# Performance work log

Hardware: AMD Instinct MI355X
Metric: run time of the kernel (lower is better)

Reference implementation:

```python
import jax, jax.numpy as jnp
import numpy as np

N, D, YD, L = 500000, 256, 50, 1000


def setup_inputs() -> dict:
    key = jax.random.key(0)
    k_x, k_l, k_y, k_w1, k_w2 = jax.random.split(key, 5)
    lim1 = 1.0 / np.sqrt(D)
    return {
        "x": jax.random.normal(k_x, (N, D), dtype=jnp.float32),
        "labels": jax.random.randint(k_l, (N,), 0, L, dtype=jnp.int32),
        "y": jax.random.uniform(k_y, (N, YD), dtype=jnp.float32),
        "w1": jax.random.uniform(k_w1, (D, 1), jnp.float32, -lim1, lim1),
        "b1": jnp.zeros((1,), jnp.float32),
        "w2": jax.random.uniform(k_w2, (D, YD), jnp.float32, -lim1, lim1),
        "b2": jnp.zeros((YD,), jnp.float32),
        "num_labels": L,
    }


def reference(x, labels, y, w1, b1, w2, b2, num_labels):
    # sigmoid-gated features: a = sigmoid(x @ w1 + b1) * x   [N, D]
    a = jax.nn.sigmoid(x @ w1 + b1) * x
    # segment counts per label (labels assumed dense 0..L-1, all present)
    counts = jax.ops.segment_sum(jnp.ones((x.shape[0],), x.dtype), labels,
                                 num_segments=num_labels)
    denom = jnp.maximum(counts, 1.0)[:, None]  # guard empty segments
    # segment mean of gated features  [L, D]
    res = jax.ops.segment_sum(a, labels, num_segments=num_labels) / denom
    # softmax(linear2(res))  [L, YD]
    prediction = jax.nn.softmax(res @ w2 + b2, axis=1)
    # segment mean of soft targets  [L, YD]
    y_mean = jax.ops.segment_sum(y, labels, num_segments=num_labels) / denom
    # torch CrossEntropyLoss with probability targets applies log_softmax
    # to its input (here: already-softmaxed prediction) -- faithful double softmax
    logp = jax.nn.log_softmax(prediction, axis=1)
    return -jnp.mean(jnp.sum(y_mean * logp, axis=1))
```

## Files before the change

### kernel.cpp

```cpp
#include <hip/hip_runtime.h>
#include <math.h>

#define NROWS 500000
#define DIM 256
#define YDIM 50
#define NLAB 1000

#define XT 64
#define NTX ((NROWS + XT - 1) / XT)
#define XBLOCKS 256
#define ASTRIDE 264
#define ZC 51

#define YT 128
#define NTY ((NROWS + YT - 1) / YT)
#define YBLOCKS 256

typedef __attribute__((ext_vector_type(8))) short frag_ab;
typedef __attribute__((ext_vector_type(4))) float frag_cd;

__device__ __forceinline__ float b2f(unsigned short u) {
    return __uint_as_float(((unsigned)u) << 16);
}
__device__ __forceinline__ unsigned short f2b(float f) {
    unsigned u = __float_as_uint(f);
    return (unsigned short)((u + 0x7fffu + ((u >> 16) & 1u)) >> 16);
}
__device__ __forceinline__ unsigned cvt_pk_bf16(float lo, float hi) {
    unsigned r;
    asm("v_cvt_pk_bf16_f32 %0, %1, %2" : "=v"(r) : "v"(lo), "v"(hi));
    return r;
}
__device__ __forceinline__ void bar_lds() {
    asm volatile("s_waitcnt lgkmcnt(0)\n\ts_barrier" ::: "memory");
}

__global__ __launch_bounds__(1024) void k_xstream(
    const float* __restrict__ x, const int* __restrict__ labels,
    const float* __restrict__ w1, const float* __restrict__ b1,
    const float* __restrict__ w2, unsigned short* __restrict__ zpart,
    float* __restrict__ out)
{
    __shared__ __align__(16) unsigned short sA[XT * ASTRIDE];
    __shared__ __align__(16) float zst[XT][52];
    __shared__ __align__(16) unsigned short accz[NLAB * YDIM];
    __shared__ int slab[2][XT];

    const int tid = threadIdx.x, lane = tid & 63, wib = tid >> 6;
    const int bid = blockIdx.x;
    const int mh = wib >> 2, jt = wib & 3;
    const int half = lane >> 5, li = lane & 31;

    if (bid == 0 && tid == 0) out[0] = 0.0f;
    for (int k = tid; k < NLAB * YDIM / 2; k += 1024)
        reinterpret_cast<unsigned*>(accz)[k] = 0u;

    frag_ab bfr[8];
    {
        const int n = 16 * jt + (lane & 15);
        #pragma unroll
        for (int s = 0; s < 8; ++s) {
            const int k0 = 32 * s + (lane >> 4) * 8;
            #pragma unroll
            for (int i = 0; i < 8; ++i) {
                const int kk = k0 + i;
                float v = 0.f;
                if (n < YDIM)       v = w2[kk * YDIM + n];
                else if (n == YDIM) v = w1[kk];
                bfr[s][i] = (short)f2b(v);
            }
        }
    }
    const float b1v = b1[0];
    __syncthreads();

    auto PREF = [&](int t, float4* r) {
        #pragma unroll
        for (int k = 0; k < 4; ++k) {
            const int rg = t * XT + 4 * wib + k;
            r[k] = (rg < NROWS)
                 ? reinterpret_cast<const float4*>(x)[(size_t)rg * 64 + lane]
                 : make_float4(0.f, 0.f, 0.f, 0.f);
        }
    };
    auto LLAB = [&](int t) -> int {
        const int rg = t * XT + tid;
        return (tid < XT && rg < NROWS) ? labels[rg] : 0;
    };

    auto process = [&](int pft, float4* r, int& lb, int par) {
        if (tid < XT) slab[par][tid] = lb;
        uint2 pk[4];
        #pragma unroll
        for (int k = 0; k < 4; ++k) {
            pk[k].x = cvt_pk_bf16(r[k].x, r[k].y);
            pk[k].y = cvt_pk_bf16(r[k].z, r[k].w);
        }
        PREF(pft, r);
        lb = LLAB(pft);
        const int row = 4 * wib;
        #pragma unroll
        for (int k = 0; k < 4; ++k)
            *reinterpret_cast<uint2*>(&sA[(row + k) * ASTRIDE + lane * 4]) = pk[k];
        bar_lds();

        frag_cd c = {0.f, 0.f, 0.f, 0.f};
        #pragma unroll
        for (int s = 0; s < 8; ++s) {
            frag_ab a = *reinterpret_cast<const frag_ab*>(
                &sA[(16 * mh + (lane & 15)) * ASTRIDE + 32 * s + (lane >> 4) * 8]);
            c = __builtin_amdgcn_mfma_f32_16x16x32_bf16(a, bfr[s], c, 0, 0, 0);
        }
        const int zr = 16 * mh + (lane >> 4) * 4;
        const int zc = 16 * jt + (lane & 15);
        if (zc < ZC) {
            zst[zr + 0][zc] = c[0]; zst[zr + 1][zc] = c[1];
            zst[zr + 2][zc] = c[2]; zst[zr + 3][zc] = c[3];
        }
        bar_lds();

        {
            const int lbl_lane = slab[par][lane];
            unsigned long long mask = __ballot((lbl_lane & 15) == wib);
            while (mask) {
                const int ra = __builtin_ctzll(mask);
                mask &= mask - 1;
                int rb = -1;
                if (mask) { rb = __builtin_ctzll(mask); mask &= mask - 1; }
                const int r2 = (half && rb >= 0) ? rb : ra;
                const int lbv = __shfl(lbl_lane, r2);
                const float d = zst[r2][YDIM];
                const bool act = (half == 0) || (rb >= 0);
                if (act && li < 25) {
                    const float g = 1.0f / (1.0f + __expf(-(d + b1v)));
                    const float2 zv =
                        *reinterpret_cast<const float2*>(&zst[r2][2 * li]);
                    unsigned* ap =
                        reinterpret_cast<unsigned*>(&accz[lbv * YDIM + 2 * li]);
                    const unsigned old = *ap;
                    const float lo = b2f((unsigned short)(old & 0xffffu)) + g * zv.x;
                    const float hi = b2f((unsigned short)(old >> 16))     + g * zv.y;
                    *ap = cvt_pk_bf16(lo, hi);
                }
            }
        }
    };

    float4 rA[4], rB[4];
    PREF(bid, rA);
    PREF(bid + XBLOCKS, rB);
    int lbA = LLAB(bid), lbB = LLAB(bid + XBLOCKS);
    int par = 0;
    for (int t = bid; t < NTX; t += 2 * XBLOCKS) {
        process(t + 2 * XBLOCKS, rA, lbA, par); par ^= 1;
        if (t + XBLOCKS < NTX) {
            process(t + 3 * XBLOCKS, rB, lbB, par); par ^= 1;
        }
    }
    __syncthreads();
    unsigned short* zp = zpart + (size_t)bid * (NLAB * YDIM);
    for (int k = tid; k < NLAB * YDIM; k += 1024) zp[k] = accz[k];
}

__global__ __launch_bounds__(1024) void k_ystream(
    const float* __restrict__ y, const int* __restrict__ labels,
    unsigned short* __restrict__ ypart, int* __restrict__ gcnt)
{
    __shared__ __align__(16) unsigned short accy[NLAB * YDIM];
    __shared__ __align__(16) float yst[2][YT * YDIM];
    __shared__ int slab[2][YT];
    __shared__ int cnt[NLAB];

    const int tid = threadIdx.x, lane = tid & 63, wib = tid >> 6;
    const int bid = blockIdx.x;
    const int half = lane >> 5, li = lane & 31;

    for (int k = tid; k < NLAB * YDIM / 2; k += 1024)
        reinterpret_cast<unsigned*>(accy)[k] = 0u;
    for (int k = tid; k < NLAB; k += 1024) cnt[k] = 0;
    __syncthreads();

    auto PREFY = [&](int t, float* v, int& myl) {
        const size_t base = (size_t)t * YT * YDIM;
        const int n = (t < NTY) ? (min(YT, NROWS - t * YT) * YDIM) : 0;
        #pragma unroll
        for (int i = 0; i < 7; ++i) {
            const int k = tid + i * 1024;
            v[i] = (k < n) ? y[base + k] : 0.f;
        }
        const int rg = t * YT + tid;
        myl = (tid < YT && t < NTY && rg < NROWS) ? labels[rg] : -1;
    };

    auto SCAT = [&](unsigned long long mask, int lblv, int ro, int par) {
        while (mask) {
            const int ra = __builtin_ctzll(mask);
            mask &= mask - 1;
            int rb = -1;
            if (mask) { rb = __builtin_ctzll(mask); mask &= mask - 1; }
            const int r2 = (half && rb >= 0) ? rb : ra;
            const int lb = __shfl(lblv, r2);
            const bool act = (half == 0) || (rb >= 0);
            if (act && li < 25) {
                const float2 yv = *reinterpret_cast<const float2*>(
                    &yst[par][(ro + r2) * YDIM + 2 * li]);
                unsigned* ap =
                    reinterpret_cast<unsigned*>(&accy[lb * YDIM + 2 * li]);
                const unsigned old = *ap;
                const float lo = b2f((unsigned short)(old & 0xffffu)) + yv.x;
                const float hi = b2f((unsigned short)(old >> 16))     + yv.y;
                *ap = cvt_pk_bf16(lo, hi);
            }
        }
    };

    auto process = [&](int pft, float* v, int& myl, int par) {
        #pragma unroll
        for (int i = 0; i < 7; ++i) {
            const int k = tid + i * 1024;
            if (k < YT * YDIM) yst[par][k] = v[i];
        }
        if (tid < YT) {
            const bool valid = (myl >= 0);
            slab[par][tid] = valid ? myl : 0;
            if (valid) atomicAdd(&cnt[myl], 1);
        }
        PREFY(pft, v, myl);
        bar_lds();

        const int l0 = slab[par][lane];
        const int l1 = slab[par][64 + lane];
        SCAT(__ballot((l0 & 15) == wib), l0, 0,  par);
        SCAT(__ballot((l1 & 15) == wib), l1, 64, par);
    };

    float vA[7], vB[7];
    int mA, mB;
    PREFY(bid, vA, mA);
    PREFY(bid + YBLOCKS, vB, mB);
    int par = 0;
    for (int t = bid; t < NTY; t += 2 * YBLOCKS) {
        process(t + 2 * YBLOCKS, vA, mA, par); par ^= 1;
        if (t + YBLOCKS < NTY) {
            process(t + 3 * YBLOCKS, vB, mB, par); par ^= 1;
        }
    }
    __syncthreads();
    unsigned short* yp = ypart + (size_t)bid * (NLAB * YDIM);
    for (int k = tid; k < NLAB * YDIM; k += 1024) yp[k] = accy[k];
    for (int k = tid; k < NLAB; k += 1024)
        if (cnt[k]) atomicAdd(&gcnt[k], cnt[k]);
}

__global__ __launch_bounds__(256) void k_finalize(
    const unsigned short* __restrict__ zpart,
    const unsigned short* __restrict__ ypart,
    const int* __restrict__ gcnt,
    const float* __restrict__ b2, float* __restrict__ out)
{
    const int tid = threadIdx.x, lane = tid & 63, grp = tid >> 6;
    const int k0 = blockIdx.x * 200;

    float zs = 0.f, ys = 0.f;
    if (tid < 200) {
        const size_t idx = (size_t)k0 + tid;
        #pragma unroll 4
        for (int p = 0; p < XBLOCKS; ++p) {
            zs += b2f(zpart[(size_t)p * (NLAB * YDIM) + idx]);
            ys += b2f(ypart[(size_t)p * (NLAB * YDIM) + idx]);
        }
    }
    __shared__ float zl[200], yl[200];
    if (tid < 200) { zl[tid] = zs; yl[tid] = ys; }
    __syncthreads();

    const int l = blockIdx.x * 4 + grp;
    const bool act = lane < YDIM;
    const float zv = act ? zl[grp * 50 + lane] : 0.f;
    const float yv = act ? yl[grp * 50 + lane] : 0.f;

    const float denom = fmaxf((float)gcnt[l], 1.0f);
    const float NEG = -3.402823466e38f;
    float logit = act ? (zv / denom + b2[lane]) : NEG;
    const float ymean = act ? (yv / denom) : 0.f;

    float m = logit;
    #pragma unroll
    for (int o = 32; o > 0; o >>= 1) m = fmaxf(m, __shfl_xor(m, o));
    float e = act ? __expf(logit - m) : 0.f;
    float s = e;
    #pragma unroll
    for (int o = 32; o > 0; o >>= 1) s += __shfl_xor(s, o);
    const float p = e / s;

    float pm = act ? p : NEG;
    float m2 = pm;
    #pragma unroll
    for (int o = 32; o > 0; o >>= 1) m2 = fmaxf(m2, __shfl_xor(m2, o));
    float e2 = act ? __expf(p - m2) : 0.f;
    float s2 = e2;
    #pragma unroll
    for (int o = 32; o > 0; o >>= 1) s2 += __shfl_xor(s2, o);
    const float logp = p - m2 - __logf(s2);

    float contrib = act ? ymean * logp : 0.f;
    #pragma unroll
    for (int o = 32; o > 0; o >>= 1) contrib += __shfl_xor(contrib, o);
    if (lane == 0) atomicAdd(out, -contrib / (float)NLAB);
}

extern "C" void kernel_launch(void* const* d_in, const int* in_sizes, int n_in,
                              void* d_out, int out_size, void* d_ws, size_t ws_size,
                              hipStream_t stream) {
    const float* x      = (const float*)d_in[0];
    const int*   labels = (const int*)  d_in[1];
    const float* y      = (const float*)d_in[2];
    const float* w1     = (const float*)d_in[3];
    const float* b1     = (const float*)d_in[4];
    const float* w2     = (const float*)d_in[5];
    const float* b2     = (const float*)d_in[6];
    float* out = (float*)d_out;

    int* gcnt = (int*)d_ws;
    unsigned short* zpart = (unsigned short*)((char*)d_ws + 4096);
    unsigned short* ypart = (unsigned short*)((char*)d_ws + 4096 +
                             (size_t)XBLOCKS * NLAB * YDIM * 2);

    hipMemsetAsync(gcnt, 0, NLAB * sizeof(int), stream);
    k_xstream<<<XBLOCKS, 1024, 0, stream>>>(x, labels, w1, b1, w2, zpart, out);
    k_ystream<<<YBLOCKS, 1024, 0, stream>>>(y, labels, ypart, gcnt);
    k_finalize<<<250, 256, 0, stream>>>(zpart, ypart, gcnt, b2, out);
}
```

Baseline: 190.2 us.

## Deepen register prefetch to three tiles and guard same-label pair scatter

Both streaming kernels now hold three tiles of prefetched registers instead of two, so global loads are issued further ahead of the LDS scatter work. The paired-row scatter loop also reads both rows' labels and only pairs them onto the two half-waves when the labels differ. If they match, the second row is left for the next iteration, which avoids two lanes doing a read-modify-write on the same bf16 accumulator at once. The deeper prefetch raises register pressure in 1024-thread blocks, and the extra shuffles and loop iterations add some scatter overhead.

```diff
diff --git a/kernel.cpp b/kernel.cpp
--- a/kernel.cpp
+++ b/kernel.cpp
@@ -125,12 +125,18 @@
             while (mask) {
                 const int ra = __builtin_ctzll(mask);
                 mask &= mask - 1;
-                int rb = -1;
-                if (mask) { rb = __builtin_ctzll(mask); mask &= mask - 1; }
-                const int r2 = (half && rb >= 0) ? rb : ra;
-                const int lbv = __shfl(lbl_lane, r2);
+                const int lba = __shfl(lbl_lane, ra);
+                int rb = -1, lbb = 0;
+                if (mask) {
+                    const int rc = __builtin_ctzll(mask);
+                    lbb = __shfl(lbl_lane, rc);
+                    if (lbb != lba) { rb = rc; mask &= mask - 1; }
+                }
+                const bool useB = (half != 0) && (rb >= 0);
+                const int r2  = useB ? rb  : ra;
+                const int lbv = useB ? lbb : lba;
+                const bool act = (half == 0) || (rb >= 0);
                 const float d = zst[r2][YDIM];
-                const bool act = (half == 0) || (rb >= 0);
                 if (act && li < 25) {
                     const float g = 1.0f / (1.0f + __expf(-(d + b1v)));
                     const float2 zv =
@@ -146,15 +152,19 @@
         }
     };
 
-    float4 rA[4], rB[4];
+    float4 rA[4], rB[4], rC[4];
     PREF(bid, rA);
     PREF(bid + XBLOCKS, rB);
-    int lbA = LLAB(bid), lbB = LLAB(bid + XBLOCKS);
+    PREF(bid + 2 * XBLOCKS, rC);
+    int lbA = LLAB(bid), lbB = LLAB(bid + XBLOCKS), lbC = LLAB(bid + 2 * XBLOCKS);
     int par = 0;
-    for (int t = bid; t < NTX; t += 2 * XBLOCKS) {
-        process(t + 2 * XBLOCKS, rA, lbA, par); par ^= 1;
+    for (int t = bid; t < NTX; t += 3 * XBLOCKS) {
+        process(t + 3 * XBLOCKS, rA, lbA, par); par ^= 1;
         if (t + XBLOCKS < NTX) {
-            process(t + 3 * XBLOCKS, rB, lbB, par); par ^= 1;
+            process(t + 4 * XBLOCKS, rB, lbB, par); par ^= 1;
+        }
+        if (t + 2 * XBLOCKS < NTX) {
+            process(t + 5 * XBLOCKS, rC, lbC, par); par ^= 1;
         }
     }
     __syncthreads();
@@ -196,10 +206,16 @@
         while (mask) {
             const int ra = __builtin_ctzll(mask);
             mask &= mask - 1;
-            int rb = -1;
-            if (mask) { rb = __builtin_ctzll(mask); mask &= mask - 1; }
-            const int r2 = (half && rb >= 0) ? rb : ra;
-            const int lb = __shfl(lblv, r2);
+            const int lba = __shfl(lblv, ra);
+            int rb = -1, lbb = 0;
+            if (mask) {
+                const int rc = __builtin_ctzll(mask);
+                lbb = __shfl(lblv, rc);
+                if (lbb != lba) { rb = rc; mask &= mask - 1; }
+            }
+            const bool useB = (half != 0) && (rb >= 0);
+            const int r2 = useB ? rb : ra;
+            const int lb = useB ? lbb : lba;
             const bool act = (half == 0) || (rb >= 0);
             if (act && li < 25) {
                 const float2 yv = *reinterpret_cast<const float2*>(
@@ -234,15 +250,19 @@
         SCAT(__ballot((l1 & 15) == wib), l1, 64, par);
     };
 
-    float vA[7], vB[7];
-    int mA, mB;
+    float vA[7], vB[7], vC[7];
+    int mA, mB, mC;
     PREFY(bid, vA, mA);
     PREFY(bid + YBLOCKS, vB, mB);
+    PREFY(bid + 2 * YBLOCKS, vC, mC);
     int par = 0;
-    for (int t = bid; t < NTY; t += 2 * YBLOCKS) {
-        process(t + 2 * YBLOCKS, vA, mA, par); par ^= 1;
+    for (int t = bid; t < NTY; t += 3 * YBLOCKS) {
+        process(t + 3 * YBLOCKS, vA, mA, par); par ^= 1;
         if (t + YBLOCKS < NTY) {
-            process(t + 3 * YBLOCKS, vB, mB, par); par ^= 1;
+            process(t + 4 * YBLOCKS, vB, mB, par); par ^= 1;
+        }
+        if (t + 2 * YBLOCKS < NTY) {
+            process(t + 5 * YBLOCKS, vC, mC, par); par ^= 1;
         }
     }
     __syncthreads();
```

Result: slower. 219.5 us (+15.4%).
